# Performance work log

Measured on AMD Instinct MI355X. Metric: run time of the kernel, lower is better.

## Reference

```python
import jax, jax.numpy as jnp
import numpy as np

K = 4
TEMPERATURE = 34.0
IN_CH = 256
OUT_CH = 256
KSIZE = 3
PAD = 1
HIDDEN = int(2 * IN_CH * 0.25) + 1  # pool_mode='mix' doubles channels -> 129


def setup_inputs() -> dict:
    key = jax.random.key(0)
    ks = jax.random.split(key, 6)
    x = jax.random.normal(ks[0], (32, IN_CH, 56, 56), dtype=jnp.float32)
    # dynamic kernel bank [K, O, C, k, k]
    weight = jax.random.normal(ks[1], (K, OUT_CH, IN_CH, KSIZE, KSIZE), dtype=jnp.float32) * 0.05
    bias_k = jnp.zeros((K, OUT_CH), dtype=jnp.float32)
    # attention MLP (1x1 convs on pooled [B, 2C, 1, 1] == linear layers)
    w1 = jax.random.normal(ks[2], (HIDDEN, 2 * IN_CH), dtype=jnp.float32) * 0.06  # fc1, no bias
    w2 = jax.random.normal(ks[3], (K, HIDDEN), dtype=jnp.float32) * 0.12
    b2 = jnp.zeros((K,), dtype=jnp.float32)
    return {"x": x, "weight": weight, "bias_k": bias_k, "w1": w1, "w2": w2, "b2": b2}


def _attention(x, w1, w2, b2):
    # mix pooling: concat(avg, max) over spatial dims -> [B, 2C]
    avg = jnp.mean(x, axis=(2, 3))
    mx = jnp.max(x, axis=(2, 3))
    p = jnp.concatenate([avg, mx], axis=1)
    h = jax.nn.relu(jnp.einsum('bc,hc->bh', p, w1))
    logits = jnp.einsum('bh,kh->bk', h, w2) + b2
    return jax.nn.softmax(logits / TEMPERATURE, axis=1)  # [B, K]


def reference(x, weight, bias_k, w1, w2, b2):
    B, C, H, W = x.shape
    attn = _attention(x, w1, w2, b2)  # [B, K]
    # per-sample aggregated kernels [B, O, C, k, k]
    agg_w = jnp.einsum('bk,kocuv->bocuv', attn, weight)
    agg_b = attn @ bias_k  # [B, O]
    # grouped-conv trick: treat batch as groups
    xg = x.reshape(1, B * C, H, W)
    wg = agg_w.reshape(B * OUT_CH, C, KSIZE, KSIZE)
    out = jax.lax.conv_general_dilated(
        xg, wg,
        window_strides=(1, 1),
        padding=[(PAD, PAD), (PAD, PAD)],
        dimension_numbers=('NCHW', 'OIHW', 'NCHW'),
        feature_group_count=B,
    )  # [1, B*O, H, W]
    out = out.reshape(B, OUT_CH, H, W) + agg_b[:, :, None, None]
    return out
```

## Files before the change

### kernel.cpp

```cpp
#include <hip/hip_runtime.h>
#include <math.h>

#define BB 32
#define CC 256
#define OO 256
#define HW 56
#define SP (HW*HW)
#define KK 4
#define HID 129
#define TEMP 34.0f
#define PROW 58
#define PLANE (PROW*PROW*32)
#define PLANEB (PROW*PROW*64)
#define NSLOT 348
#define QSLOT 350
#define QSTRIDE (QSLOT*16)
#define NPIECE (4*QSLOT)
#define BUFB (4*QSTRIDE)

typedef unsigned short u16;
typedef unsigned int uint32;
typedef __attribute__((ext_vector_type(8))) short bf16x8;
typedef __attribute__((ext_vector_type(4))) float f32x4;

__device__ __forceinline__ u16 f2bf(float f) {
    union { float f; uint32 u; } v; v.f = f;
    uint32 r = v.u + 0x7FFF + ((v.u >> 16) & 1);
    return (u16)(r >> 16);
}

__device__ __forceinline__ void gload16(const void* g, void* l) {
    __builtin_amdgcn_global_load_lds(
        (const __attribute__((address_space(1))) unsigned int*)g,
        (__attribute__((address_space(3))) unsigned int*)l, 16, 0, 0);
}

__global__ __launch_bounds__(256) void trans_pool(const float* __restrict__ x,
                                                  u16* __restrict__ xt,
                                                  float* __restrict__ pooled) {
    const int cb = blockIdx.x, b = blockIdx.y;
    const int tid = threadIdx.x;
    const int lane = tid & 63, wave = tid >> 6;
    const float* xp = x + ((size_t)b * CC + cb * 32) * SP;
    u16* xtb = xt + (size_t)(b * 8 + cb) * PLANE;

    if (tid < 228) {
        int slot;
        if (tid < 58)       slot = tid;
        else if (tid < 116) slot = 57 * 58 + (tid - 58);
        else if (tid < 172) slot = (tid - 116 + 1) * 58;
        else                slot = (tid - 172 + 1) * 58 + 57;
        bf16x8 z = {};
        #pragma unroll
        for (int j = 0; j < 4; ++j)
            *(bf16x8*)&xtb[(size_t)slot * 32 + j * 8] = z;
    }

    float psum[32], pmax[32];
    #pragma unroll
    for (int c = 0; c < 32; ++c) { psum[c] = 0.f; pmax[c] = -INFINITY; }

    for (int p0 = 0; p0 < SP; p0 += 256) {
        const int p = p0 + tid;
        const bool v = p < SP;
        const int pc = v ? p : (SP - 1);
        u16 ob[32];
        #pragma unroll
        for (int c = 0; c < 32; ++c) {
            const float vv = xp[(size_t)c * SP + pc];
            if (v) { psum[c] += vv; pmax[c] = fmaxf(pmax[c], vv); }
            ob[c] = f2bf(vv);
        }
        if (v) {
            const int slot = (p / 56 + 1) * 58 + (p % 56 + 1);
            #pragma unroll
            for (int j = 0; j < 4; ++j)
                *(bf16x8*)&xtb[(size_t)slot * 32 + j * 8] = *(bf16x8*)&ob[j * 8];
        }
    }
    #pragma unroll
    for (int c = 0; c < 32; ++c) {
        #pragma unroll
        for (int off = 32; off >= 1; off >>= 1) {
            psum[c] += __shfl_xor(psum[c], off, 64);
            pmax[c] = fmaxf(pmax[c], __shfl_xor(pmax[c], off, 64));
        }
    }
    __shared__ float ssum[4][32];
    __shared__ float smax[4][32];
    if (lane == 0) {
        #pragma unroll
        for (int c = 0; c < 32; ++c) { ssum[wave][c] = psum[c]; smax[wave][c] = pmax[c]; }
    }
    __syncthreads();
    if (tid < 32) {
        const float s = ssum[0][tid] + ssum[1][tid] + ssum[2][tid] + ssum[3][tid];
        const float m = fmaxf(fmaxf(smax[0][tid], smax[1][tid]),
                              fmaxf(smax[2][tid], smax[3][tid]));
        pooled[b * (2 * CC) + cb * 32 + tid]      = s / (float)SP;
        pooled[b * (2 * CC) + CC + cb * 32 + tid] = m;
    }
}

__global__ __launch_bounds__(256) void attn_kernel(const float* __restrict__ pooled,
                                                   const float* __restrict__ w1,
                                                   const float* __restrict__ w2,
                                                   const float* __restrict__ b2,
                                                   const float* __restrict__ bias_k,
                                                   float* __restrict__ attn,
                                                   float* __restrict__ agg_b) {
    const int b = blockIdx.x;
    const int tid = threadIdx.x;
    __shared__ float p[2 * CC];
    __shared__ float h[HID];
    __shared__ float a[KK];
    for (int i = tid; i < 2 * CC; i += 256) p[i] = pooled[b * 2 * CC + i];
    __syncthreads();
    if (tid < HID) {
        float s = 0.f;
        const float* w1r = w1 + (size_t)tid * (2 * CC);
        for (int c = 0; c < 2 * CC; ++c) s = fmaf(p[c], w1r[c], s);
        h[tid] = fmaxf(s, 0.f);
    }
    __syncthreads();
    if (tid == 0) {
        float lg[KK];
        float m = -INFINITY;
        for (int k = 0; k < KK; ++k) {
            float s = b2[k];
            for (int i = 0; i < HID; ++i) s = fmaf(h[i], w2[k * HID + i], s);
            lg[k] = s / TEMP;
            m = fmaxf(m, lg[k]);
        }
        float den = 0.f;
        for (int k = 0; k < KK; ++k) { lg[k] = expf(lg[k] - m); den += lg[k]; }
        for (int k = 0; k < KK; ++k) { a[k] = lg[k] / den; attn[b * KK + k] = a[k]; }
    }
    __syncthreads();
    if (tid < OO) {
        float s = 0.f;
        #pragma unroll
        for (int k = 0; k < KK; ++k) s = fmaf(a[k], bias_k[k * OO + tid], s);
        agg_b[b * OO + tid] = s;
    }
}

__global__ __launch_bounds__(256) void agg_kernel(const float* __restrict__ weight,
                                                  const float* __restrict__ attn,
                                                  u16* __restrict__ wT) {
    const int o = blockIdx.x;
    const int c = threadIdx.x;
    __shared__ float at[BB * KK];
    if (threadIdx.x < BB * KK) at[threadIdx.x] = attn[threadIdx.x];
    __syncthreads();
    float w[KK][9];
    #pragma unroll
    for (int k = 0; k < KK; ++k)
        #pragma unroll
        for (int uv = 0; uv < 9; ++uv)
            w[k][uv] = weight[(size_t)((k * OO + o) * CC + c) * 9 + uv];
    for (int b = 0; b < BB; ++b) {
        const float a0 = at[b*KK+0], a1 = at[b*KK+1], a2 = at[b*KK+2], a3 = at[b*KK+3];
        #pragma unroll
        for (int uv = 0; uv < 9; ++uv) {
            float s = a0 * w[0][uv] + a1 * w[1][uv] + a2 * w[2][uv] + a3 * w[3][uv];
            wT[(size_t)((b * 9 + uv) * OO + o) * CC + c] = f2bf(s);
        }
    }
}

__global__ __launch_bounds__(512, 4) void conv_mfma(const u16* __restrict__ xt,
                                                    const u16* __restrict__ wT,
                                                    const float* __restrict__ agg_b,
                                                    float* __restrict__ out) {
    const int id   = blockIdx.x;
    const int g    = id >> 3;
    const int b    = (id & 7) + 8 * (g / 28);
    const int tile = g % 28;
    const int px   = tile % 14, oy = tile / 14;
    const int tid  = threadIdx.x;
    const int lane = tid & 63, wave = tid >> 6;
    const int wm = wave & 3, wn = wave >> 2;
    const int l15 = lane & 15, kg = lane >> 4;
    const int p0 = px * 224;

    __shared__ char xs[2][BUFB];

    uint32 soff[3]; bool sact[3];
    #pragma unroll
    for (int k = 0; k < 3; ++k) {
        const int i = k * 512 + tid;
        sact[k] = (i < NPIECE);
        const int q = i / QSLOT, slot = i % QSLOT;
        soff[k] = (uint32)((px * 232 + slot) * 64 + q * 16);
    }

    int bboff[7];
    #pragma unroll
    for (int nf = 0; nf < 7; ++nf) {
        const int n = wn * 112 + nf * 16 + l15;
        const int S = (n / 56 + 1) * 58 + (n % 56 + 1);
        bboff[nf] = kg * QSTRIDE + S * 16;
    }

    const u16* wTb = wT + (size_t)b * 9 * OO * CC
                        + (size_t)(oy * 128 + wm * 32 + l15) * CC + kg * 8;

    f32x4 acc[2][7];
    #pragma unroll
    for (int mf = 0; mf < 2; ++mf)
        #pragma unroll
        for (int nf = 0; nf < 7; ++nf)
            acc[mf][nf] = (f32x4)0.f;

    const char* xgb = (const char*)xt + (size_t)(b * 8) * PLANEB;

    #pragma unroll
    for (int k = 0; k < 3; ++k)
        if (sact[k]) gload16(xgb + soff[k], &xs[0][k * 8192 + wave * 1024]);
    __syncthreads();

    for (int cb = 0; cb < 8; ++cb) {
        const char* R = xs[cb & 1];
        char* W = xs[(cb & 1) ^ 1];
        const char* xg_next = xgb + (size_t)(cb + 1) * PLANEB;
        const int c0 = cb * 32;

        #pragma unroll
        for (int uv = 0; uv < 9; ++uv) {
            if (uv < 3 && cb < 7) {
                if (sact[uv]) gload16(xg_next + soff[uv], &W[uv * 8192 + wave * 1024]);
            }
            bf16x8 av[2];
            #pragma unroll
            for (int mf = 0; mf < 2; ++mf)
                av[mf] = *(const bf16x8*)(wTb + (size_t)uv * OO * CC + mf * 16 * CC + c0);
            const int dby = ((uv / 3 - 1) * 58 + (uv % 3 - 1)) * 16;
            __builtin_amdgcn_s_setprio(1);
            #pragma unroll
            for (int nf = 0; nf < 7; ++nf) {
                const bf16x8 bv = *(const bf16x8*)(R + bboff[nf] + dby);
                #pragma unroll
                for (int mf = 0; mf < 2; ++mf)
                    acc[mf][nf] = __builtin_amdgcn_mfma_f32_16x16x32_bf16(av[mf], bv, acc[mf][nf], 0, 0, 0);
            }
            __builtin_amdgcn_s_setprio(0);
        }
        __syncthreads();
    }

    const int obase = oy * 128 + wm * 32;
    float* outb = out + (size_t)b * OO * SP;
    #pragma unroll
    for (int mf = 0; mf < 2; ++mf) {
        #pragma unroll
        for (int r = 0; r < 4; ++r) {
            const int o = obase + mf * 16 + kg * 4 + r;
            const float bias = agg_b[b * OO + o];
            #pragma unroll
            for (int nf = 0; nf < 7; ++nf) {
                const int p = p0 + wn * 112 + nf * 16 + l15;
                outb[(size_t)o * SP + p] = acc[mf][nf][r] + bias;
            }
        }
    }
}

extern "C" void kernel_launch(void* const* d_in, const int* in_sizes, int n_in,
                              void* d_out, int out_size, void* d_ws, size_t ws_size,
                              hipStream_t stream) {
    const float* x      = (const float*)d_in[0];
    const float* weight = (const float*)d_in[1];
    const float* bias_k = (const float*)d_in[2];
    const float* w1     = (const float*)d_in[3];
    const float* w2     = (const float*)d_in[4];
    const float* b2     = (const float*)d_in[5];
    float* out = (float*)d_out;

    u16* x_t = (u16*)d_ws;
    u16* wT  = x_t + (size_t)BB * 8 * PLANE;
    float* ws_f   = (float*)(wT + (size_t)BB * 9 * OO * CC);
    float* pooled = ws_f;
    float* attn   = ws_f + BB * 2 * CC;
    float* agg_b  = attn + BB * KK;

    trans_pool<<<dim3(8, BB), 256, 0, stream>>>(x, x_t, pooled);
    attn_kernel<<<BB, 256, 0, stream>>>(pooled, w1, w2, b2, bias_k, attn, agg_b);
    agg_kernel<<<OO, 256, 0, stream>>>(weight, attn, wT);
    conv_mfma<<<896, 512, 0, stream>>>(x_t, wT, agg_b, out);
}
```

Measured before the change: 232.3 us.

## Stage aggregated weights through LDS with triple-buffered async pipeline in conv

The aggregation kernel now writes the per-sample bf16 weights in a tiled layout, with one contiguous 8 KB region per (b, uv, channel block, output half). The conv kernel streams these regions into a triple-buffered LDS ring with global_load_lds, instead of loading them directly from global memory per wave. The input planes stay double-buffered. Synchronisation uses manual vmcnt waits plus a barrier on every tap, replacing the per-block __syncthreads. This is meant to hide the latency of A-operand loads and overlap copies with MFMA work, at the cost of more LDS use and a barrier per tap, which may hurt occupancy.

```diff
diff --git a/kernel.cpp b/kernel.cpp
--- a/kernel.cpp
+++ b/kernel.cpp
@@ -16,12 +16,16 @@
 #define QSLOT 350
 #define QSTRIDE (QSLOT*16)
 #define NPIECE (4*QSLOT)
-#define BUFB (4*QSTRIDE)
+#define XA_B 8192
+#define XB_B 24576
 
 typedef unsigned short u16;
 typedef unsigned int uint32;
 typedef __attribute__((ext_vector_type(8))) short bf16x8;
 typedef __attribute__((ext_vector_type(4))) float f32x4;
+
+#define WAITVM(n) asm volatile("s_waitcnt vmcnt(" #n ")" ::: "memory")
+#define WAITLGKM() asm volatile("s_waitcnt lgkmcnt(0)" ::: "memory")
 
 __device__ __forceinline__ u16 f2bf(float f) {
     union { float f; uint32 u; } v; v.f = f;
@@ -147,7 +151,7 @@
 
 __global__ __launch_bounds__(256) void agg_kernel(const float* __restrict__ weight,
                                                   const float* __restrict__ attn,
-                                                  u16* __restrict__ wT) {
+                                                  u16* __restrict__ wT2) {
     const int o = blockIdx.x;
     const int c = threadIdx.x;
     __shared__ float at[BB * KK];
@@ -159,18 +163,22 @@
         #pragma unroll
         for (int uv = 0; uv < 9; ++uv)
             w[k][uv] = weight[(size_t)((k * OO + o) * CC + c) * 9 + uv];
+    const int cb = c >> 5, kg = (c >> 3) & 3, cl = c & 7;
+    const int oy = o >> 7, ol = o & 127;
+    const size_t sub = (size_t)kg * 1024 + ol * 8 + cl;
     for (int b = 0; b < BB; ++b) {
         const float a0 = at[b*KK+0], a1 = at[b*KK+1], a2 = at[b*KK+2], a3 = at[b*KK+3];
         #pragma unroll
         for (int uv = 0; uv < 9; ++uv) {
             float s = a0 * w[0][uv] + a1 * w[1][uv] + a2 * w[2][uv] + a3 * w[3][uv];
-            wT[(size_t)((b * 9 + uv) * OO + o) * CC + c] = f2bf(s);
+            const size_t region = (((size_t)b * 9 + uv) * 8 + cb) * 2 + oy;
+            wT2[region * 4096 + sub] = f2bf(s);
         }
     }
 }
 
 __global__ __launch_bounds__(512, 4) void conv_mfma(const u16* __restrict__ xt,
-                                                    const u16* __restrict__ wT,
+                                                    const u16* __restrict__ wT2,
                                                     const float* __restrict__ agg_b,
                                                     float* __restrict__ out) {
     const int id   = blockIdx.x;
@@ -184,13 +192,14 @@
     const int l15 = lane & 15, kg = lane >> 4;
     const int p0 = px * 224;
 
-    __shared__ char xs[2][BUFB];
-
-    uint32 soff[3]; bool sact[3];
+    __shared__ char XA[3][XA_B];
+    __shared__ char XB[2][XB_B];
+
+    uint32 soff[3];
     #pragma unroll
     for (int k = 0; k < 3; ++k) {
-        const int i = k * 512 + tid;
-        sact[k] = (i < NPIECE);
+        int i = k * 512 + tid;
+        if (i >= NPIECE) i = NPIECE - 1;
         const int q = i / QSLOT, slot = i % QSLOT;
         soff[k] = (uint32)((px * 232 + slot) * 64 + q * 16);
     }
@@ -203,8 +212,13 @@
         bboff[nf] = kg * QSTRIDE + S * 16;
     }
 
-    const u16* wTb = wT + (size_t)b * 9 * OO * CC
-                        + (size_t)(oy * 128 + wm * 32 + l15) * CC + kg * 8;
+    const int aoff0 = kg * 2048 + (wm * 32 + l15) * 16;
+    const int aoff1 = aoff0 + 16 * 16;
+
+    const char* xgb = (const char*)xt + (size_t)(b * 8) * PLANEB;
+    const char* wAb = (const char*)wT2 + (size_t)b * 9 * 8 * 2 * 8192
+                     + (size_t)oy * 8192;
+    const size_t tb = (size_t)tid * 16;
 
     f32x4 acc[2][7];
     #pragma unroll
@@ -213,40 +227,52 @@
         for (int nf = 0; nf < 7; ++nf)
             acc[mf][nf] = (f32x4)0.f;
 
-    const char* xgb = (const char*)xt + (size_t)(b * 8) * PLANEB;
-
     #pragma unroll
     for (int k = 0; k < 3; ++k)
-        if (sact[k]) gload16(xgb + soff[k], &xs[0][k * 8192 + wave * 1024]);
-    __syncthreads();
+        gload16(xgb + soff[k], &XB[0][k * 8192 + wave * 1024]);
+    gload16(wAb + (size_t)(0 * 8 + 0) * 2 * 8192 + tb, &XA[0][wave * 1024]);
+    gload16(wAb + (size_t)(1 * 8 + 0) * 2 * 8192 + tb, &XA[1][wave * 1024]);
 
     for (int cb = 0; cb < 8; ++cb) {
-        const char* R = xs[cb & 1];
-        char* W = xs[(cb & 1) ^ 1];
-        const char* xg_next = xgb + (size_t)(cb + 1) * PLANEB;
-        const int c0 = cb * 32;
+        const char* RB = XB[cb & 1];
+        char* WB = XB[(cb & 1) ^ 1];
+        const char* xg_next = xgb + (size_t)((cb + 1) & 7) * PLANEB;
 
         #pragma unroll
         for (int uv = 0; uv < 9; ++uv) {
-            if (uv < 3 && cb < 7) {
-                if (sact[uv]) gload16(xg_next + soff[uv], &W[uv * 8192 + wave * 1024]);
+            if (uv == 2 || uv == 3) WAITVM(3);
+            else if (uv == 1 || uv == 4) WAITVM(2);
+            else WAITVM(1);
+            __builtin_amdgcn_s_barrier();
+
+            const char* RA = XA[uv % 3];
+            bf16x8 av0 = *(const bf16x8*)(RA + aoff0);
+            bf16x8 av1 = *(const bf16x8*)(RA + aoff1);
+            const int dby = ((uv / 3 - 1) * 58 + (uv % 3 - 1)) * 16;
+            bf16x8 bv[7];
+            #pragma unroll
+            for (int nf = 0; nf < 7; ++nf)
+                bv[nf] = *(const bf16x8*)(RB + bboff[nf] + dby);
+
+            {
+                const int uv_s = (uv + 2 < 9) ? uv + 2 : uv - 7;
+                const int cb_s = (uv + 2 < 9) ? cb : ((cb + 1) & 7);
+                gload16(wAb + (size_t)(uv_s * 8 + cb_s) * 2 * 8192 + tb,
+                        &XA[(uv + 2) % 3][wave * 1024]);
             }
-            bf16x8 av[2];
-            #pragma unroll
-            for (int mf = 0; mf < 2; ++mf)
-                av[mf] = *(const bf16x8*)(wTb + (size_t)uv * OO * CC + mf * 16 * CC + c0);
-            const int dby = ((uv / 3 - 1) * 58 + (uv % 3 - 1)) * 16;
+            if (uv < 3)
+                gload16(xg_next + soff[uv], &WB[uv * 8192 + wave * 1024]);
+
+            WAITLGKM();
+            __builtin_amdgcn_sched_barrier(0);
             __builtin_amdgcn_s_setprio(1);
             #pragma unroll
             for (int nf = 0; nf < 7; ++nf) {
-                const bf16x8 bv = *(const bf16x8*)(R + bboff[nf] + dby);
-                #pragma unroll
-                for (int mf = 0; mf < 2; ++mf)
-                    acc[mf][nf] = __builtin_amdgcn_mfma_f32_16x16x32_bf16(av[mf], bv, acc[mf][nf], 0, 0, 0);
+                acc[0][nf] = __builtin_amdgcn_mfma_f32_16x16x32_bf16(av0, bv[nf], acc[0][nf], 0, 0, 0);
+                acc[1][nf] = __builtin_amdgcn_mfma_f32_16x16x32_bf16(av1, bv[nf], acc[1][nf], 0, 0, 0);
             }
             __builtin_amdgcn_s_setprio(0);
         }
-        __syncthreads();
     }
 
     const int obase = oy * 128 + wm * 32;
@@ -278,14 +304,14 @@
     float* out = (float*)d_out;
 
     u16* x_t = (u16*)d_ws;
-    u16* wT  = x_t + (size_t)BB * 8 * PLANE;
-    float* ws_f   = (float*)(wT + (size_t)BB * 9 * OO * CC);
+    u16* wT2 = x_t + (size_t)BB * 8 * PLANE;
+    float* ws_f   = (float*)(wT2 + (size_t)BB * 9 * OO * CC);
     float* pooled = ws_f;
     float* attn   = ws_f + BB * 2 * CC;
     float* agg_b  = attn + BB * KK;
 
     trans_pool<<<dim3(8, BB), 256, 0, stream>>>(x, x_t, pooled);
     attn_kernel<<<BB, 256, 0, stream>>>(pooled, w1, w2, b2, bias_k, attn, agg_b);
-    agg_kernel<<<OO, 256, 0, stream>>>(weight, attn, wT);
-    conv_mfma<<<896, 512, 0, stream>>>(x_t, wT, agg_b, out);
-}
+    agg_kernel<<<OO, 256, 0, stream>>>(weight, attn, wT2);
+    conv_mfma<<<896, 512, 0, stream>>>(x_t, wT2, agg_b, out);
+}
```

Result: faster. 207.0 us (-10.9%).
